# Kernel tuning notes

Hardware: AMD Instinct MI355X
Metric: run time of the kernel (lower is better)

## Reference

```python
import jax, jax.numpy as jnp
import numpy as np

NG, NT, E = 2500, 20000, 640000
SRC_DIM, DST_DIM, HID, OUT, NCLS = 128, 500, 128, 128, 16


def setup_inputs() -> dict:
    key = jax.random.key(0)
    ks = jax.random.split(key, 11)
    d = {
        "gene_feats": jax.random.normal(ks[0], (NG, SRC_DIM), jnp.float32),
        "train_feats": jax.random.normal(ks[1], (NT, DST_DIM), jnp.float32),
        "edge_src": jax.random.randint(ks[2], (E,), 0, NG),
        "edge_dst": jax.random.randint(ks[3], (E,), 0, NT),
        # conv1: SAGEConv((src_dim, dst_dim) -> hidden)
        "W1_neigh": jax.random.normal(ks[4], (SRC_DIM, HID), jnp.float32) / np.sqrt(SRC_DIM),
        "W1_self": jax.random.normal(ks[5], (DST_DIM, HID), jnp.float32) / np.sqrt(DST_DIM),
        "b1": jnp.zeros((HID,), jnp.float32),
        # conv2: SAGEConv(hidden -> out); src input is the raw gene features
        "W2_neigh": jax.random.normal(ks[6], (HID, OUT), jnp.float32) / np.sqrt(HID),
        "W2_self": jax.random.normal(ks[7], (HID, OUT), jnp.float32) / np.sqrt(HID),
        "b2": jnp.zeros((OUT,), jnp.float32),
        # classifier MLP
        "Wc1": jax.random.normal(ks[8], (OUT, OUT), jnp.float32) / np.sqrt(OUT),
        "bc1": jnp.zeros((OUT,), jnp.float32),
        "Wc2": jax.random.normal(ks[9], (OUT, NCLS), jnp.float32) / np.sqrt(OUT),
        "bc2": jnp.zeros((NCLS,), jnp.float32),
    }
    return d


def _segment_mean(msgs, dst, num_segments):
    # mean over in-edges; isolated dst nodes get 0 (DGL convention)
    sums = jax.ops.segment_sum(msgs, dst, num_segments=num_segments)
    cnt = jax.ops.segment_sum(jnp.ones((msgs.shape[0],), msgs.dtype), dst,
                              num_segments=num_segments)
    return sums / jnp.maximum(cnt, 1.0)[:, None]


def reference(gene_feats, train_feats, edge_src, edge_dst,
              W1_neigh, W1_self, b1, W2_neigh, W2_self, b2,
              Wc1, bc1, Wc2, bc2):
    # mean-aggregate gene (src) features onto train (dst) nodes
    agg = _segment_mean(gene_feats[edge_src], edge_dst, NT)  # [NT, SRC_DIM]
    # conv1: fc_self(h_dst) + fc_neigh(mean_neigh) + bias, then ReLU
    h1 = jax.nn.relu(train_feats @ W1_self + agg @ W1_neigh + b1)  # [NT, HID]
    # conv2 reuses raw gene features as src -> same mean aggregation
    h2 = jax.nn.relu(h1 @ W2_self + agg @ W2_neigh + b2)  # [NT, OUT]
    # classifier: Linear -> ReLU -> Linear
    return jax.nn.relu(h2 @ Wc1 + bc1) @ Wc2 + bc2  # [NT, NCLS]
```

## Files before the change

### kernel.cpp

```cpp
#include <hip/hip_runtime.h>


#define NG 2500
#define NT 20000
#define NE 640000
#define NCLS 16
#define CAP 96
#define NTILE 1250

typedef unsigned short u16;
typedef unsigned int u32;

typedef float f32x4 __attribute__((ext_vector_type(4)));
typedef __bf16 bf16x8 __attribute__((ext_vector_type(8)));

__device__ __forceinline__ float b2f(u16 u) { return __uint_as_float(((u32)u) << 16); }
__device__ __forceinline__ float blo(u32 p) { return __uint_as_float(p << 16); }
__device__ __forceinline__ float bhi(u32 p) { return __uint_as_float(p & 0xffff0000u); }
__device__ __forceinline__ u16 f2b(float f) {
    u32 u = __float_as_uint(f);
    return (u16)((u + 0x7fffu + ((u >> 16) & 1u)) >> 16);
}

#define B1N 81920
#define B2N 32768
#define B3N 16384
#define B4N 2048
#define CVB NTILE
#define GNB 625
#define PKB 520

__global__ __launch_bounds__(256) void k_edges(const int* __restrict__ esrc,
                                               const int* __restrict__ edst,
                                               int* __restrict__ cnt,
                                               u16* __restrict__ csr) {
    int e = blockIdx.x * 256 + threadIdx.x;
    if (e < NE) {
        unsigned d = (unsigned)edst[e];
        if (d < NT) {
            int slot = atomicAdd(&cnt[d], 1);
            if (slot < CAP) csr[(size_t)d * CAP + slot] = (u16)esrc[e];
        }
    }
}

__global__ __launch_bounds__(256) void k_conv(
    const float* __restrict__ train, const float* __restrict__ gene,
    u16* __restrict__ AF, u32* __restrict__ GH32,
    const float* __restrict__ W1n, const float* __restrict__ W1s,
    const float* __restrict__ W2n, const float* __restrict__ W2s,
    const float* __restrict__ Wc1, const float* __restrict__ Wc2,
    u16* __restrict__ B1h, u16* __restrict__ B1l,
    u16* __restrict__ B2h, u16* __restrict__ B2l,
    u16* __restrict__ B3h, u16* __restrict__ B3l,
    u16* __restrict__ B4h, u16* __restrict__ B4l) {
    int blk = blockIdx.x, t = threadIdx.x;
    if (blk < CVB) {
        __shared__ __align__(16) u16 L[16 * 520];
        u32* L32 = (u32*)L;
        int tile = blk;
        for (int i = t; i < 160; i += 256) {
            int r = i / 10, c = i - r * 10;
            L32[r * 260 + 250 + c] = 0;
        }
        for (int i = t; i < 2000; i += 256) {
            int r = i / 125, c4 = i - r * 125;
            float4 v = *(const float4*)(train + (size_t)(tile * 16 + r) * 500 + c4 * 4);
            int base = r * 260 + c4 * 2;
            L32[base] = (u32)f2b(v.x) | ((u32)f2b(v.y) << 16);
            L32[base + 1] = (u32)f2b(v.z) | ((u32)f2b(v.w) << 16);
        }
        __syncthreads();
#pragma unroll
        for (int it = 0; it < 4; ++it) {
            int slot = t + it * 256;
            int kk = slot >> 6, lane = slot & 63;
            int m = lane & 15, q = lane >> 4;
            uint4 v = *(const uint4*)(L + m * 520 + kk * 32 + q * 8);
            *(uint4*)(AF + (((size_t)tile * 16 + kk) * 64 + lane) * 8) = v;
        }
        return;
    }
    if (blk < CVB + GNB) {
        int idx = (blk - CVB) * 256 + t;
        float2 v = ((const float2*)gene)[idx];
        GH32[idx] = (u32)f2b(v.x) | ((u32)f2b(v.y) << 16);
        return;
    }
    int idx = (blk - CVB - GNB) * 256 + t;
    float v = 0.f;
    u16 *ph = 0, *pl = 0;
    int off = 0;
    if (idx < B1N) {
        int j = idx & 7, l = (idx >> 3) & 63, rest = idx >> 9;
        int g = rest & 7, kk = rest >> 3;
        int k = kk * 32 + ((l >> 4) << 3) + j, n = (g << 4) + (l & 15);
        if (k < 500) v = W1s[k * 128 + n];
        else if (k >= 512) v = W1n[(k - 512) * 128 + n];
        ph = B1h; pl = B1l; off = idx;
    } else if (idx < B1N + B2N) {
        int e = idx - B1N;
        int j = e & 7, l = (e >> 3) & 63, rest = e >> 9;
        int g = rest & 7, kk = rest >> 3;
        int k = kk * 32 + ((l >> 4) << 3) + j, n = (g << 4) + (l & 15);
        v = (k < 128) ? W2s[k * 128 + n] : W2n[(k - 128) * 128 + n];
        ph = B2h; pl = B2l; off = e;
    } else if (idx < B1N + B2N + B3N) {
        int e = idx - (B1N + B2N);
        int j = e & 7, l = (e >> 3) & 63, rest = e >> 9;
        int g = rest & 7, kk = rest >> 3;
        int k = kk * 32 + ((l >> 4) << 3) + j, n = (g << 4) + (l & 15);
        v = Wc1[k * 128 + n];
        ph = B3h; pl = B3l; off = e;
    } else if (idx < B1N + B2N + B3N + B4N) {
        int e = idx - (B1N + B2N + B3N);
        int j = e & 7, l = (e >> 3) & 63, kk = e >> 9;
        int k = kk * 32 + ((l >> 4) << 3) + j, n = l & 15;
        v = Wc2[k * 16 + n];
        ph = B4h; pl = B4l; off = e;
    }
    if (ph) {
        u16 hi = f2b(v);
        u16 lo = f2b(v - b2f(hi));
        ph[off] = hi;
        pl[off] = lo;
    }
}

__global__ __launch_bounds__(512) void k_mega(
    const int* __restrict__ cnt, const u16* __restrict__ csr,
    const u16* __restrict__ GH, const u16* __restrict__ AF,
    const u16* __restrict__ B1h, const u16* __restrict__ B1l,
    const u16* __restrict__ B2h, const u16* __restrict__ B2l,
    const u16* __restrict__ B3h, const u16* __restrict__ B3l,
    const u16* __restrict__ B4h, const u16* __restrict__ B4l,
    const float* __restrict__ b1, const float* __restrict__ b2,
    const float* __restrict__ bc1, const float* __restrict__ bc2,
    float* __restrict__ out) {
    __shared__ __align__(16) u16 SAGh[32 * 136], SAGl[32 * 136];
    __shared__ __align__(16) u16 S1h[32 * 136], S1l[32 * 136];
    __shared__ __align__(16) u16 S2h[32 * 136], S2l[32 * 136];
    int t = threadIdx.x;
    int row0 = blockIdx.x * 32;

    {
        int r = t >> 4, cg = t & 15;
        int d = row0 + r;
        int ctrue = cnt[d];
        int c = ctrue > CAP ? CAP : ctrue;
        const u16* crow = csr + (size_t)d * CAP;
        float a[8];
#pragma unroll
        for (int p = 0; p < 8; ++p) a[p] = 0.f;
        int j = 0;
        for (; j + 1 < c; j += 2) {
            int s0 = crow[j], s1 = crow[j + 1];
            uint4 p0 = *(const uint4*)(GH + (size_t)s0 * 128 + cg * 8);
            uint4 p1 = *(const uint4*)(GH + (size_t)s1 * 128 + cg * 8);
            a[0] += blo(p0.x); a[1] += bhi(p0.x);
            a[2] += blo(p0.y); a[3] += bhi(p0.y);
            a[4] += blo(p0.z); a[5] += bhi(p0.z);
            a[6] += blo(p0.w); a[7] += bhi(p0.w);
            a[0] += blo(p1.x); a[1] += bhi(p1.x);
            a[2] += blo(p1.y); a[3] += bhi(p1.y);
            a[4] += blo(p1.z); a[5] += bhi(p1.z);
            a[6] += blo(p1.w); a[7] += bhi(p1.w);
        }
        if (j < c) {
            int s = crow[j];
            uint4 p0 = *(const uint4*)(GH + (size_t)s * 128 + cg * 8);
            a[0] += blo(p0.x); a[1] += bhi(p0.x);
            a[2] += blo(p0.y); a[3] += bhi(p0.y);
            a[4] += blo(p0.z); a[5] += bhi(p0.z);
            a[6] += blo(p0.w); a[7] += bhi(p0.w);
        }
        float inv = (ctrue > 0) ? 1.f / (float)ctrue : 0.f;
        int base = (r * 136 + cg * 8) >> 1;
        u32* SH = (u32*)SAGh;
        u32* SL = (u32*)SAGl;
#pragma unroll
        for (int p = 0; p < 4; ++p) {
            float x = a[2 * p] * inv, y = a[2 * p + 1] * inv;
            u16 hx = f2b(x), hy = f2b(y);
            SH[base + p] = (u32)hx | ((u32)hy << 16);
            SL[base + p] = (u32)f2b(x - b2f(hx)) | ((u32)f2b(y - b2f(hy)) << 16);
        }
    }
    __syncthreads();

    int lane = t & 63, wave = t >> 6;
    int rt = wave & 1, cw = wave >> 1;
    int g0 = cw * 2;
    int m = lane & 15, q = lane >> 4, n16 = lane & 15;
    int tile = blockIdx.x * 2 + rt;

    const u16* aBase = AF + (((size_t)tile * 16) * 64 + lane) * 8;
    int hrow = (rt * 16 + m) * 136 + q * 8;
    int crow = rt * 16 + q * 4;
    const f32x4 z4 = {0.f, 0.f, 0.f, 0.f};
    f32x4 acc0 = z4, acc1 = z4;

#pragma unroll 4
    for (int kk = 0; kk < 16; ++kk) {
        bf16x8 ah = *(const bf16x8*)(aBase + kk * 512);
        size_t bo0 = ((size_t)(kk * 8 + g0) * 64 + lane) * 8;
        bf16x8 bh0 = *(const bf16x8*)(B1h + bo0);
        bf16x8 bl0 = *(const bf16x8*)(B1l + bo0);
        bf16x8 bh1 = *(const bf16x8*)(B1h + bo0 + 512);
        bf16x8 bl1 = *(const bf16x8*)(B1l + bo0 + 512);
        acc0 = __builtin_amdgcn_mfma_f32_16x16x32_bf16(ah, bh0, acc0, 0, 0, 0);
        acc0 = __builtin_amdgcn_mfma_f32_16x16x32_bf16(ah, bl0, acc0, 0, 0, 0);
        acc1 = __builtin_amdgcn_mfma_f32_16x16x32_bf16(ah, bh1, acc1, 0, 0, 0);
        acc1 = __builtin_amdgcn_mfma_f32_16x16x32_bf16(ah, bl1, acc1, 0, 0, 0);
    }
#pragma unroll
    for (int kk = 16; kk < 20; ++kk) {
        bf16x8 ah = *(const bf16x8*)(SAGh + hrow + (kk - 16) * 32);
        bf16x8 al = *(const bf16x8*)(SAGl + hrow + (kk - 16) * 32);
        size_t bo0 = ((size_t)(kk * 8 + g0) * 64 + lane) * 8;
        bf16x8 bh0 = *(const bf16x8*)(B1h + bo0);
        bf16x8 bl0 = *(const bf16x8*)(B1l + bo0);
        bf16x8 bh1 = *(const bf16x8*)(B1h + bo0 + 512);
        bf16x8 bl1 = *(const bf16x8*)(B1l + bo0 + 512);
        acc0 = __builtin_amdgcn_mfma_f32_16x16x32_bf16(ah, bh0, acc0, 0, 0, 0);
        acc0 = __builtin_amdgcn_mfma_f32_16x16x32_bf16(ah, bl0, acc0, 0, 0, 0);
        acc0 = __builtin_amdgcn_mfma_f32_16x16x32_bf16(al, bh0, acc0, 0, 0, 0);
        acc1 = __builtin_amdgcn_mfma_f32_16x16x32_bf16(ah, bh1, acc1, 0, 0, 0);
        acc1 = __builtin_amdgcn_mfma_f32_16x16x32_bf16(ah, bl1, acc1, 0, 0, 0);
        acc1 = __builtin_amdgcn_mfma_f32_16x16x32_bf16(al, bh1, acc1, 0, 0, 0);
    }
    {
        int n0 = g0 * 16 + n16, n1 = n0 + 16;
        float bias0 = b1[n0], bias1 = b1[n1];
#pragma unroll
        for (int rg = 0; rg < 4; ++rg) {
            float v0 = acc0[rg] + bias0; v0 = v0 > 0.f ? v0 : 0.f;
            float v1 = acc1[rg] + bias1; v1 = v1 > 0.f ? v1 : 0.f;
            u16 h0 = f2b(v0), h1v = f2b(v1);
            int ix = (crow + rg) * 136;
            S1h[ix + n0] = h0; S1l[ix + n0] = f2b(v0 - b2f(h0));
            S1h[ix + n1] = h1v; S1l[ix + n1] = f2b(v1 - b2f(h1v));
        }
    }
    __syncthreads();

    acc0 = z4; acc1 = z4;
#pragma unroll
    for (int kk = 0; kk < 8; ++kk) {
        bf16x8 ah, al;
        if (kk < 4) {
            ah = *(const bf16x8*)(S1h + hrow + kk * 32);
            al = *(const bf16x8*)(S1l + hrow + kk * 32);
        } else {
            ah = *(const bf16x8*)(SAGh + hrow + (kk - 4) * 32);
            al = *(const bf16x8*)(SAGl + hrow + (kk - 4) * 32);
        }
        size_t bo0 = ((size_t)(kk * 8 + g0) * 64 + lane) * 8;
        bf16x8 bh0 = *(const bf16x8*)(B2h + bo0);
        bf16x8 bl0 = *(const bf16x8*)(B2l + bo0);
        bf16x8 bh1 = *(const bf16x8*)(B2h + bo0 + 512);
        bf16x8 bl1 = *(const bf16x8*)(B2l + bo0 + 512);
        acc0 = __builtin_amdgcn_mfma_f32_16x16x32_bf16(ah, bh0, acc0, 0, 0, 0);
        acc0 = __builtin_amdgcn_mfma_f32_16x16x32_bf16(ah, bl0, acc0, 0, 0, 0);
        acc0 = __builtin_amdgcn_mfma_f32_16x16x32_bf16(al, bh0, acc0, 0, 0, 0);
        acc1 = __builtin_amdgcn_mfma_f32_16x16x32_bf16(ah, bh1, acc1, 0, 0, 0);
        acc1 = __builtin_amdgcn_mfma_f32_16x16x32_bf16(ah, bl1, acc1, 0, 0, 0);
        acc1 = __builtin_amdgcn_mfma_f32_16x16x32_bf16(al, bh1, acc1, 0, 0, 0);
    }
    {
        int n0 = g0 * 16 + n16, n1 = n0 + 16;
        float bias0 = b2[n0], bias1 = b2[n1];
#pragma unroll
        for (int rg = 0; rg < 4; ++rg) {
            float v0 = acc0[rg] + bias0; v0 = v0 > 0.f ? v0 : 0.f;
            float v1 = acc1[rg] + bias1; v1 = v1 > 0.f ? v1 : 0.f;
            u16 h0 = f2b(v0), h1v = f2b(v1);
            int ix = (crow + rg) * 136;
            S2h[ix + n0] = h0; S2l[ix + n0] = f2b(v0 - b2f(h0));
            S2h[ix + n1] = h1v; S2l[ix + n1] = f2b(v1 - b2f(h1v));
        }
    }
    __syncthreads();

    acc0 = z4; acc1 = z4;
#pragma unroll
    for (int kk = 0; kk < 4; ++kk) {
        bf16x8 ah = *(const bf16x8*)(S2h + hrow + kk * 32);
        bf16x8 al = *(const bf16x8*)(S2l + hrow + kk * 32);
        size_t bo0 = ((size_t)(kk * 8 + g0) * 64 + lane) * 8;
        bf16x8 bh0 = *(const bf16x8*)(B3h + bo0);
        bf16x8 bl0 = *(const bf16x8*)(B3l + bo0);
        bf16x8 bh1 = *(const bf16x8*)(B3h + bo0 + 512);
        bf16x8 bl1 = *(const bf16x8*)(B3l + bo0 + 512);
        acc0 = __builtin_amdgcn_mfma_f32_16x16x32_bf16(ah, bh0, acc0, 0, 0, 0);
        acc0 = __builtin_amdgcn_mfma_f32_16x16x32_bf16(ah, bl0, acc0, 0, 0, 0);
        acc0 = __builtin_amdgcn_mfma_f32_16x16x32_bf16(al, bh0, acc0, 0, 0, 0);
        acc1 = __builtin_amdgcn_mfma_f32_16x16x32_bf16(ah, bh1, acc1, 0, 0, 0);
        acc1 = __builtin_amdgcn_mfma_f32_16x16x32_bf16(ah, bl1, acc1, 0, 0, 0);
        acc1 = __builtin_amdgcn_mfma_f32_16x16x32_bf16(al, bh1, acc1, 0, 0, 0);
    }
    {
        int n0 = g0 * 16 + n16, n1 = n0 + 16;
        float bias0 = bc1[n0], bias1 = bc1[n1];
#pragma unroll
        for (int rg = 0; rg < 4; ++rg) {
            float v0 = acc0[rg] + bias0; v0 = v0 > 0.f ? v0 : 0.f;
            float v1 = acc1[rg] + bias1; v1 = v1 > 0.f ? v1 : 0.f;
            u16 h0 = f2b(v0), h1v = f2b(v1);
            int ix = (crow + rg) * 136;
            S1h[ix + n0] = h0; S1l[ix + n0] = f2b(v0 - b2f(h0));
            S1h[ix + n1] = h1v; S1l[ix + n1] = f2b(v1 - b2f(h1v));
        }
    }
    __syncthreads();

    if (cw == 0) {
        f32x4 a4 = z4;
#pragma unroll
        for (int kk = 0; kk < 4; ++kk) {
            bf16x8 ah = *(const bf16x8*)(S1h + hrow + kk * 32);
            bf16x8 al = *(const bf16x8*)(S1l + hrow + kk * 32);
            size_t bo = ((size_t)kk * 64 + lane) * 8;
            bf16x8 bh = *(const bf16x8*)(B4h + bo);
            bf16x8 bl = *(const bf16x8*)(B4l + bo);
            a4 = __builtin_amdgcn_mfma_f32_16x16x32_bf16(ah, bh, a4, 0, 0, 0);
            a4 = __builtin_amdgcn_mfma_f32_16x16x32_bf16(ah, bl, a4, 0, 0, 0);
            a4 = __builtin_amdgcn_mfma_f32_16x16x32_bf16(al, bh, a4, 0, 0, 0);
        }
        float bias = bc2[n16];
#pragma unroll
        for (int rg = 0; rg < 4; ++rg)
            out[(size_t)(row0 + crow + rg) * NCLS + n16] = a4[rg] + bias;
    }
}

extern "C" void kernel_launch(void* const* d_in, const int* in_sizes, int n_in,
                              void* d_out, int out_size, void* d_ws, size_t ws_size,
                              hipStream_t stream) {
    const float* gene = (const float*)d_in[0];
    const float* train = (const float*)d_in[1];
    const int* esrc = (const int*)d_in[2];
    const int* edst = (const int*)d_in[3];

    char* ws = (char*)d_ws;
    int* cnt = (int*)(ws + 0);
    u16* csr = (u16*)(ws + 80000);
    u16* AF = (u16*)(ws + 3920000);
    u16* GH = (u16*)(ws + 24400000);
    u16* B1h = (u16*)(ws + 25040000);
    u16* B1l = (u16*)(ws + 25203840);
    u16* B2h = (u16*)(ws + 25367680);
    u16* B2l = (u16*)(ws + 25433216);
    u16* B3h = (u16*)(ws + 25498752);
    u16* B3l = (u16*)(ws + 25531520);
    u16* B4h = (u16*)(ws + 25564288);
    u16* B4l = (u16*)(ws + 25568384);

    hipMemsetAsync(cnt, 0, NT * sizeof(int), stream);
    k_edges<<<(NE + 255) / 256, 256, 0, stream>>>(esrc, edst, cnt, csr);
    k_conv<<<CVB + GNB + PKB, 256, 0, stream>>>(
        train, gene, AF, (u32*)GH,
        (const float*)d_in[4], (const float*)d_in[5], (const float*)d_in[7],
        (const float*)d_in[8], (const float*)d_in[10], (const float*)d_in[12],
        B1h, B1l, B2h, B2l, B3h, B3l, B4h, B4l);
    k_mega<<<NT / 32, 512, 0, stream>>>(
        cnt, csr, GH, AF, B1h, B1l, B2h, B2l, B3h, B3l, B4h, B4l,
        (const float*)d_in[6], (const float*)d_in[9], (const float*)d_in[11],
        (const float*)d_in[13], (float*)d_out);
}
```

Baseline: 186.2 us.

## Merge edge-CSR build into prep kernel and remap waves to share B fragments

Folds the edge-bucketing kernel into the preprocessing kernel as extra blocks, removing one launch and letting edge scatter overlap with feature and weight conversion. In the fused main kernel, each wave now owns one 16-column group across both 16-row tiles instead of two column groups for one tile. Each wave therefore loads one B fragment pair per k-step and reuses it across two A tiles, halving global weight-fragment loads per wave while doubling the A/LDS reads. The final classifier stage now runs on waves 0 and 1, one per row tile.

Result: faster. 179.1 us (-3.8%).

```diff
diff --git a/kernel.cpp b/kernel.cpp
--- a/kernel.cpp
+++ b/kernel.cpp
@@ -26,25 +26,14 @@
 #define B2N 32768
 #define B3N 16384
 #define B4N 2048
+#define NEB 2500
 #define CVB NTILE
 #define GNB 625
 #define PKB 520
 
-__global__ __launch_bounds__(256) void k_edges(const int* __restrict__ esrc,
-                                               const int* __restrict__ edst,
-                                               int* __restrict__ cnt,
-                                               u16* __restrict__ csr) {
-    int e = blockIdx.x * 256 + threadIdx.x;
-    if (e < NE) {
-        unsigned d = (unsigned)edst[e];
-        if (d < NT) {
-            int slot = atomicAdd(&cnt[d], 1);
-            if (slot < CAP) csr[(size_t)d * CAP + slot] = (u16)esrc[e];
-        }
-    }
-}
-
-__global__ __launch_bounds__(256) void k_conv(
+__global__ __launch_bounds__(256) void k_prep(
+    const int* __restrict__ esrc, const int* __restrict__ edst,
+    int* __restrict__ cnt, u16* __restrict__ csr,
     const float* __restrict__ train, const float* __restrict__ gene,
     u16* __restrict__ AF, u32* __restrict__ GH32,
     const float* __restrict__ W1n, const float* __restrict__ W1s,
@@ -55,10 +44,21 @@
     u16* __restrict__ B3h, u16* __restrict__ B3l,
     u16* __restrict__ B4h, u16* __restrict__ B4l) {
     int blk = blockIdx.x, t = threadIdx.x;
-    if (blk < CVB) {
+    if (blk < NEB) {
+        int e = blk * 256 + t;
+        if (e < NE) {
+            unsigned d = (unsigned)edst[e];
+            if (d < NT) {
+                int slot = atomicAdd(&cnt[d], 1);
+                if (slot < CAP) csr[(size_t)d * CAP + slot] = (u16)esrc[e];
+            }
+        }
+        return;
+    }
+    if (blk < NEB + CVB) {
         __shared__ __align__(16) u16 L[16 * 520];
         u32* L32 = (u32*)L;
-        int tile = blk;
+        int tile = blk - NEB;
         for (int i = t; i < 160; i += 256) {
             int r = i / 10, c = i - r * 10;
             L32[r * 260 + 250 + c] = 0;
@@ -81,13 +81,13 @@
         }
         return;
     }
-    if (blk < CVB + GNB) {
-        int idx = (blk - CVB) * 256 + t;
+    if (blk < NEB + CVB + GNB) {
+        int idx = (blk - NEB - CVB) * 256 + t;
         float2 v = ((const float2*)gene)[idx];
         GH32[idx] = (u32)f2b(v.x) | ((u32)f2b(v.y) << 16);
         return;
     }
-    int idx = (blk - CVB - GNB) * 256 + t;
+    int idx = (blk - NEB - CVB - GNB) * 256 + t;
     float v = 0.f;
     u16 *ph = 0, *pl = 0;
     int off = 0;
@@ -188,58 +188,57 @@
     }
     __syncthreads();
 
-    int lane = t & 63, wave = t >> 6;
-    int rt = wave & 1, cw = wave >> 1;
-    int g0 = cw * 2;
+    int lane = t & 63, g = t >> 6;
     int m = lane & 15, q = lane >> 4, n16 = lane & 15;
-    int tile = blockIdx.x * 2 + rt;
-
-    const u16* aBase = AF + (((size_t)tile * 16) * 64 + lane) * 8;
-    int hrow = (rt * 16 + m) * 136 + q * 8;
-    int crow = rt * 16 + q * 4;
+    size_t tile0 = (size_t)blockIdx.x * 2;
+
+    const u16* aB0 = AF + ((tile0 * 16) * 64 + lane) * 8;
+    const u16* aB1 = AF + (((tile0 + 1) * 16) * 64 + lane) * 8;
+    int hr0 = m * 136 + q * 8;
+    int hr1 = (16 + m) * 136 + q * 8;
+    int cr0 = q * 4, cr1 = 16 + q * 4;
     const f32x4 z4 = {0.f, 0.f, 0.f, 0.f};
     f32x4 acc0 = z4, acc1 = z4;
 
 #pragma unroll 4
     for (int kk = 0; kk < 16; ++kk) {
-        bf16x8 ah = *(const bf16x8*)(aBase + kk * 512);
-        size_t bo0 = ((size_t)(kk * 8 + g0) * 64 + lane) * 8;
-        bf16x8 bh0 = *(const bf16x8*)(B1h + bo0);
-        bf16x8 bl0 = *(const bf16x8*)(B1l + bo0);
-        bf16x8 bh1 = *(const bf16x8*)(B1h + bo0 + 512);
-        bf16x8 bl1 = *(const bf16x8*)(B1l + bo0 + 512);
-        acc0 = __builtin_amdgcn_mfma_f32_16x16x32_bf16(ah, bh0, acc0, 0, 0, 0);
-        acc0 = __builtin_amdgcn_mfma_f32_16x16x32_bf16(ah, bl0, acc0, 0, 0, 0);
-        acc1 = __builtin_amdgcn_mfma_f32_16x16x32_bf16(ah, bh1, acc1, 0, 0, 0);
-        acc1 = __builtin_amdgcn_mfma_f32_16x16x32_bf16(ah, bl1, acc1, 0, 0, 0);
+        bf16x8 a0 = *(const bf16x8*)(aB0 + kk * 512);
+        bf16x8 a1 = *(const bf16x8*)(aB1 + kk * 512);
+        size_t bo = ((size_t)(kk * 8 + g) * 64 + lane) * 8;
+        bf16x8 bh = *(const bf16x8*)(B1h + bo);
+        bf16x8 bl = *(const bf16x8*)(B1l + bo);
+        acc0 = __builtin_amdgcn_mfma_f32_16x16x32_bf16(a0, bh, acc0, 0, 0, 0);
+        acc0 = __builtin_amdgcn_mfma_f32_16x16x32_bf16(a0, bl, acc0, 0, 0, 0);
+        acc1 = __builtin_amdgcn_mfma_f32_16x16x32_bf16(a1, bh, acc1, 0, 0, 0);
+        acc1 = __builtin_amdgcn_mfma_f32_16x16x32_bf16(a1, bl, acc1, 0, 0, 0);
     }
 #pragma unroll
     for (int kk = 16; kk < 20; ++kk) {
-        bf16x8 ah = *(const bf16x8*)(SAGh + hrow + (kk - 16) * 32);
-        bf16x8 al = *(const bf16x8*)(SAGl + hrow + (kk - 16) * 32);
-        size_t bo0 = ((size_t)(kk * 8 + g0) * 64 + lane) * 8;
-        bf16x8 bh0 = *(const bf16x8*)(B1h + bo0);
-        bf16x8 bl0 = *(const bf16x8*)(B1l + bo0);
-        bf16x8 bh1 = *(const bf16x8*)(B1h + bo0 + 512);
-        bf16x8 bl1 = *(const bf16x8*)(B1l + bo0 + 512);
-        acc0 = __builtin_amdgcn_mfma_f32_16x16x32_bf16(ah, bh0, acc0, 0, 0, 0);
-        acc0 = __builtin_amdgcn_mfma_f32_16x16x32_bf16(ah, bl0, acc0, 0, 0, 0);
-        acc0 = __builtin_amdgcn_mfma_f32_16x16x32_bf16(al, bh0, acc0, 0, 0, 0);
-        acc1 = __builtin_amdgcn_mfma_f32_16x16x32_bf16(ah, bh1, acc1, 0, 0, 0);
-        acc1 = __builtin_amdgcn_mfma_f32_16x16x32_bf16(ah, bl1, acc1, 0, 0, 0);
-        acc1 = __builtin_amdgcn_mfma_f32_16x16x32_bf16(al, bh1, acc1, 0, 0, 0);
+        int o = (kk - 16) * 32;
+        bf16x8 ah0 = *(const bf16x8*)(SAGh + hr0 + o);
+        bf16x8 al0 = *(const bf16x8*)(SAGl + hr0 + o);
+        bf16x8 ah1 = *(const bf16x8*)(SAGh + hr1 + o);
+        bf16x8 al1 = *(const bf16x8*)(SAGl + hr1 + o);
+        size_t bo = ((size_t)(kk * 8 + g) * 64 + lane) * 8;
+        bf16x8 bh = *(const bf16x8*)(B1h + bo);
+        bf16x8 bl = *(const bf16x8*)(B1l + bo);
+        acc0 = __builtin_amdgcn_mfma_f32_16x16x32_bf16(ah0, bh, acc0, 0, 0, 0);
+        acc0 = __builtin_amdgcn_mfma_f32_16x16x32_bf16(ah0, bl, acc0, 0, 0, 0);
+        acc0 = __builtin_amdgcn_mfma_f32_16x16x32_bf16(al0, bh, acc0, 0, 0, 0);
+        acc1 = __builtin_amdgcn_mfma_f32_16x16x32_bf16(ah1, bh, acc1, 0, 0, 0);
+        acc1 = __builtin_amdgcn_mfma_f32_16x16x32_bf16(ah1, bl, acc1, 0, 0, 0);
+        acc1 = __builtin_amdgcn_mfma_f32_16x16x32_bf16(al1, bh, acc1, 0, 0, 0);
     }
     {
-        int n0 = g0 * 16 + n16, n1 = n0 + 16;
-        float bias0 = b1[n0], bias1 = b1[n1];
+        int n = g * 16 + n16;
+        float bias = b1[n];
 #pragma unroll
         for (int rg = 0; rg < 4; ++rg) {
-            float v0 = acc0[rg] + bias0; v0 = v0 > 0.f ? v0 : 0.f;
-            float v1 = acc1[rg] + bias1; v1 = v1 > 0.f ? v1 : 0.f;
+            float v0 = acc0[rg] + bias; v0 = v0 > 0.f ? v0 : 0.f;
+            float v1 = acc1[rg] + bias; v1 = v1 > 0.f ? v1 : 0.f;
             u16 h0 = f2b(v0), h1v = f2b(v1);
-            int ix = (crow + rg) * 136;
-            S1h[ix + n0] = h0; S1l[ix + n0] = f2b(v0 - b2f(h0));
-            S1h[ix + n1] = h1v; S1l[ix + n1] = f2b(v1 - b2f(h1v));
+            S1h[(cr0 + rg) * 136 + n] = h0; S1l[(cr0 + rg) * 136 + n] = f2b(v0 - b2f(h0));
+            S1h[(cr1 + rg) * 136 + n] = h1v; S1l[(cr1 + rg) * 136 + n] = f2b(v1 - b2f(h1v));
         }
     }
     __syncthreads();
@@ -247,37 +246,33 @@
     acc0 = z4; acc1 = z4;
 #pragma unroll
     for (int kk = 0; kk < 8; ++kk) {
-        bf16x8 ah, al;
-        if (kk < 4) {
-            ah = *(const bf16x8*)(S1h + hrow + kk * 32);
-            al = *(const bf16x8*)(S1l + hrow + kk * 32);
-        } else {
-            ah = *(const bf16x8*)(SAGh + hrow + (kk - 4) * 32);
-            al = *(const bf16x8*)(SAGl + hrow + (kk - 4) * 32);
-        }
-        size_t bo0 = ((size_t)(kk * 8 + g0) * 64 + lane) * 8;
-        bf16x8 bh0 = *(const bf16x8*)(B2h + bo0);
-        bf16x8 bl0 = *(const bf16x8*)(B2l + bo0);
-        bf16x8 bh1 = *(const bf16x8*)(B2h + bo0 + 512);
-        bf16x8 bl1 = *(const bf16x8*)(B2l + bo0 + 512);
-        acc0 = __builtin_amdgcn_mfma_f32_16x16x32_bf16(ah, bh0, acc0, 0, 0, 0);
-        acc0 = __builtin_amdgcn_mfma_f32_16x16x32_bf16(ah, bl0, acc0, 0, 0, 0);
-        acc0 = __builtin_amdgcn_mfma_f32_16x16x32_bf16(al, bh0, acc0, 0, 0, 0);
-        acc1 = __builtin_amdgcn_mfma_f32_16x16x32_bf16(ah, bh1, acc1, 0, 0, 0);
-        acc1 = __builtin_amdgcn_mfma_f32_16x16x32_bf16(ah, bl1, acc1, 0, 0, 0);
-        acc1 = __builtin_amdgcn_mfma_f32_16x16x32_bf16(al, bh1, acc1, 0, 0, 0);
+        const u16* Ph = (kk < 4) ? S1h : SAGh;
+        const u16* Pl = (kk < 4) ? S1l : SAGl;
+        int o = (kk & 3) * 32;
+        bf16x8 ah0 = *(const bf16x8*)(Ph + hr0 + o);
+        bf16x8 al0 = *(const bf16x8*)(Pl + hr0 + o);
+        bf16x8 ah1 = *(const bf16x8*)(Ph + hr1 + o);
+        bf16x8 al1 = *(const bf16x8*)(Pl + hr1 + o);
+        size_t bo = ((size_t)(kk * 8 + g) * 64 + lane) * 8;
+        bf16x8 bh = *(const bf16x8*)(B2h + bo);
+        bf16x8 bl = *(const bf16x8*)(B2l + bo);
+        acc0 = __builtin_amdgcn_mfma_f32_16x16x32_bf16(ah0, bh, acc0, 0, 0, 0);
+        acc0 = __builtin_amdgcn_mfma_f32_16x16x32_bf16(ah0, bl, acc0, 0, 0, 0);
+        acc0 = __builtin_amdgcn_mfma_f32_16x16x32_bf16(al0, bh, acc0, 0, 0, 0);
+        acc1 = __builtin_amdgcn_mfma_f32_16x16x32_bf16(ah1, bh, acc1, 0, 0, 0);
+        acc1 = __builtin_amdgcn_mfma_f32_16x16x32_bf16(ah1, bl, acc1, 0, 0, 0);
+        acc1 = __builtin_amdgcn_mfma_f32_16x16x32_bf16(al1, bh, acc1, 0, 0, 0);
     }
     {
-        int n0 = g0 * 16 + n16, n1 = n0 + 16;
-        float bias0 = b2[n0], bias1 = b2[n1];
+        int n = g * 16 + n16;
+        float bias = b2[n];
 #pragma unroll
         for (int rg = 0; rg < 4; ++rg) {
-            float v0 = acc0[rg] + bias0; v0 = v0 > 0.f ? v0 : 0.f;
-            float v1 = acc1[rg] + bias1; v1 = v1 > 0.f ? v1 : 0.f;
+            float v0 = acc0[rg] + bias; v0 = v0 > 0.f ? v0 : 0.f;
+            float v1 = acc1[rg] + bias; v1 = v1 > 0.f ? v1 : 0.f;
             u16 h0 = f2b(v0), h1v = f2b(v1);
-            int ix = (crow + rg) * 136;
-            S2h[ix + n0] = h0; S2l[ix + n0] = f2b(v0 - b2f(h0));
-            S2h[ix + n1] = h1v; S2l[ix + n1] = f2b(v1 - b2f(h1v));
+            S2h[(cr0 + rg) * 136 + n] = h0; S2l[(cr0 + rg) * 136 + n] = f2b(v0 - b2f(h0));
+            S2h[(cr1 + rg) * 136 + n] = h1v; S2l[(cr1 + rg) * 136 + n] = f2b(v1 - b2f(h1v));
         }
     }
     __syncthreads();
@@ -285,41 +280,43 @@
     acc0 = z4; acc1 = z4;
 #pragma unroll
     for (int kk = 0; kk < 4; ++kk) {
-        bf16x8 ah = *(const bf16x8*)(S2h + hrow + kk * 32);
-        bf16x8 al = *(const bf16x8*)(S2l + hrow + kk * 32);
-        size_t bo0 = ((size_t)(kk * 8 + g0) * 64 + lane) * 8;
-        bf16x8 bh0 = *(const bf16x8*)(B3h + bo0);
-        bf16x8 bl0 = *(const bf16x8*)(B3l + bo0);
-        bf16x8 bh1 = *(const bf16x8*)(B3h + bo0 + 512);
-        bf16x8 bl1 = *(const bf16x8*)(B3l + bo0 + 512);
-        acc0 = __builtin_amdgcn_mfma_f32_16x16x32_bf16(ah, bh0, acc0, 0, 0, 0);
-        acc0 = __builtin_amdgcn_mfma_f32_16x16x32_bf16(ah, bl0, acc0, 0, 0, 0);
-        acc0 = __builtin_amdgcn_mfma_f32_16x16x32_bf16(al, bh0, acc0, 0, 0, 0);
-        acc1 = __builtin_amdgcn_mfma_f32_16x16x32_bf16(ah, bh1, acc1, 0, 0, 0);
-        acc1 = __builtin_amdgcn_mfma_f32_16x16x32_bf16(ah, bl1, acc1, 0, 0, 0);
-        acc1 = __builtin_amdgcn_mfma_f32_16x16x32_bf16(al, bh1, acc1, 0, 0, 0);
+        int o = kk * 32;
+        bf16x8 ah0 = *(const bf16x8*)(S2h + hr0 + o);
+        bf16x8 al0 = *(const bf16x8*)(S2l + hr0 + o);
+        bf16x8 ah1 = *(const bf16x8*)(S2h + hr1 + o);
+        bf16x8 al1 = *(const bf16x8*)(S2l + hr1 + o);
+        size_t bo = ((size_t)(kk * 8 + g) * 64 + lane) * 8;
+        bf16x8 bh = *(const bf16x8*)(B3h + bo);
+        bf16x8 bl = *(const bf16x8*)(B3l + bo);
+        acc0 = __builtin_amdgcn_mfma_f32_16x16x32_bf16(ah0, bh, acc0, 0, 0, 0);
+        acc0 = __builtin_amdgcn_mfma_f32_16x16x32_bf16(ah0, bl, acc0, 0, 0, 0);
+        acc0 = __builtin_amdgcn_mfma_f32_16x16x32_bf16(al0, bh, acc0, 0, 0, 0);
+        acc1 = __builtin_amdgcn_mfma_f32_16x16x32_bf16(ah1, bh, acc1, 0, 0, 0);
+        acc1 = __builtin_amdgcn_mfma_f32_16x16x32_bf16(ah1, bl, acc1, 0, 0, 0);
+        acc1 = __builtin_amdgcn_mfma_f32_16x16x32_bf16(al1, bh, acc1, 0, 0, 0);
     }
     {
-        int n0 = g0 * 16 + n16, n1 = n0 + 16;
-        float bias0 = bc1[n0], bias1 = bc1[n1];
+        int n = g * 16 + n16;
+        float bias = bc1[n];
 #pragma unroll
         for (int rg = 0; rg < 4; ++rg) {
-            float v0 = acc0[rg] + bias0; v0 = v0 > 0.f ? v0 : 0.f;
-            float v1 = acc1[rg] + bias1; v1 = v1 > 0.f ? v1 : 0.f;
+            float v0 = acc0[rg] + bias; v0 = v0 > 0.f ? v0 : 0.f;
+            float v1 = acc1[rg] + bias; v1 = v1 > 0.f ? v1 : 0.f;
             u16 h0 = f2b(v0), h1v = f2b(v1);
-            int ix = (crow + rg) * 136;
-            S1h[ix + n0] = h0; S1l[ix + n0] = f2b(v0 - b2f(h0));
-            S1h[ix + n1] = h1v; S1l[ix + n1] = f2b(v1 - b2f(h1v));
+            S1h[(cr0 + rg) * 136 + n] = h0; S1l[(cr0 + rg) * 136 + n] = f2b(v0 - b2f(h0));
+            S1h[(cr1 + rg) * 136 + n] = h1v; S1l[(cr1 + rg) * 136 + n] = f2b(v1 - b2f(h1v));
         }
     }
     __syncthreads();
 
-    if (cw == 0) {
+    if (g < 2) {
+        int hr = (g == 0) ? hr0 : hr1;
+        int cr = (g == 0) ? cr0 : cr1;
         f32x4 a4 = z4;
 #pragma unroll
         for (int kk = 0; kk < 4; ++kk) {
-            bf16x8 ah = *(const bf16x8*)(S1h + hrow + kk * 32);
-            bf16x8 al = *(const bf16x8*)(S1l + hrow + kk * 32);
+            bf16x8 ah = *(const bf16x8*)(S1h + hr + kk * 32);
+            bf16x8 al = *(const bf16x8*)(S1l + hr + kk * 32);
             size_t bo = ((size_t)kk * 64 + lane) * 8;
             bf16x8 bh = *(const bf16x8*)(B4h + bo);
             bf16x8 bl = *(const bf16x8*)(B4l + bo);
@@ -330,7 +327,7 @@
         float bias = bc2[n16];
 #pragma unroll
         for (int rg = 0; rg < 4; ++rg)
-            out[(size_t)(row0 + crow + rg) * NCLS + n16] = a4[rg] + bias;
+            out[(size_t)(row0 + cr + rg) * NCLS + n16] = a4[rg] + bias;
     }
 }
 
@@ -357,9 +354,8 @@
     u16* B4l = (u16*)(ws + 25568384);
 
     hipMemsetAsync(cnt, 0, NT * sizeof(int), stream);
-    k_edges<<<(NE + 255) / 256, 256, 0, stream>>>(esrc, edst, cnt, csr);
-    k_conv<<<CVB + GNB + PKB, 256, 0, stream>>>(
-        train, gene, AF, (u32*)GH,
+    k_prep<<<NEB + CVB + GNB + PKB, 256, 0, stream>>>(
+        esrc, edst, cnt, csr, train, gene, AF, (u32*)GH,
         (const float*)d_in[4], (const float*)d_in[5], (const float*)d_in[7],
         (const float*)d_in[8], (const float*)d_in[10], (const float*)d_in[12],
         B1h, B1l, B2h, B2l, B3h, B3l, B4h, B4l);
```
